# Kernel tuning notes

Measured on AMD Instinct MI355X. Metric: run time of the kernel, lower is better.

## Reference

```python
import jax, jax.numpy as jnp
import numpy as np

N_HEADS = 18
HEAD_DIM = 16
ROPE_THETA = 10000.0
SLIDING_WINDOW = 4096


def _rotate_half(x):
    half = x.shape[-1] // 2
    return jnp.concatenate([-x[..., half:], x[..., :half]], axis=-1)


def setup_inputs() -> dict:
    key = jax.random.key(0)
    k0, k1, k2, k3, k4 = jax.random.split(key, 5)
    B, S, H = 2, 2048, 288
    std = 0.02
    return {
        "hidden_states": jax.random.normal(k0, (B, S, H), dtype=jnp.float32),
        "Wq": jax.random.normal(k1, (H, H), dtype=jnp.float32) * std,
        "Wk": jax.random.normal(k2, (H, H), dtype=jnp.float32) * std,
        "Wv": jax.random.normal(k3, (H, H), dtype=jnp.float32) * std,
        "Wo": jax.random.normal(k4, (H, H), dtype=jnp.float32) * std,
    }


def reference(hidden_states, Wq, Wk, Wv, Wo):
    B, S, H = hidden_states.shape
    nH, D = N_HEADS, HEAD_DIM

    # QKV projections (nn.Linear: y = x @ W.T), reshape to [B, nH, S, D]
    def proj(W):
        return jnp.einsum("bsh,oh->bso", hidden_states, W).reshape(B, S, nH, D).transpose(0, 2, 1, 3)

    q, k, v = proj(Wq), proj(Wk), proj(Wv)

    # Rotary embedding: position_ids = arange(S)
    pos = jnp.arange(S, dtype=jnp.float32)
    inv_freq = 1.0 / (ROPE_THETA ** (jnp.arange(0, D, 2, dtype=jnp.float32) / D))
    freqs = pos[:, None] * inv_freq[None, :]            # [S, D/2]
    emb = jnp.concatenate([freqs, freqs], axis=-1)      # [S, D]
    cos = jnp.cos(emb)[None, None, :, :]                # [1, 1, S, D]
    sin = jnp.sin(emb)[None, None, :, :]
    q = q * cos + _rotate_half(q) * sin
    k = k * cos + _rotate_half(k) * sin

    # num_key_value_groups = 1 -> repeat_kv is identity.
    scores = jnp.einsum("bhqd,bhkd->bhqk", q, k) / jnp.sqrt(jnp.float32(D))

    # Sliding-window causal mask: attend iff 0 <= i - j < window
    i = jnp.arange(S)[:, None]
    j = jnp.arange(S)[None, :]
    allowed = (j <= i) & (i - j < SLIDING_WINDOW)       # [S, S]
    neg = jnp.finfo(scores.dtype).min
    scores = jnp.where(allowed[None, None, :, :], scores, neg)

    attn = jax.nn.softmax(scores.astype(jnp.float32), axis=-1).astype(q.dtype)
    out = jnp.einsum("bhqk,bhkd->bhqd", attn, v)        # [B, nH, S, D]
    out = out.transpose(0, 2, 1, 3).reshape(B, S, H)
    return jnp.einsum("bsh,oh->bso", out, Wo)
```

## Files before the change

kernel.cpp:

```cpp
#include <hip/hip_runtime.h>
#include <hip/hip_bf16.h>
#include <math.h>

#define H_DIM 288
#define NHEADS 18
#define HEAD_D 16
#define SEQ 2048
#define BATCH 2
#define M_TOT (BATCH*SEQ)
#define XCNT (M_TOT*H_DIM)
#define WCNT (H_DIM*H_DIM)

typedef _Float16 f16_t;
typedef __attribute__((ext_vector_type(4))) _Float16 half4v;
typedef __attribute__((ext_vector_type(8))) _Float16 half8v;
typedef __attribute__((ext_vector_type(4))) float   float4v;

__global__ __launch_bounds__(256) void cvt_f16(
    const float* __restrict__ X,
    const float* __restrict__ Wq, const float* __restrict__ Wk,
    const float* __restrict__ Wv, const float* __restrict__ Wo,
    f16_t* __restrict__ Xf, f16_t* __restrict__ Wf)
{
    int idx = blockIdx.x * 256 + threadIdx.x;
    const int X4 = XCNT/4, W4 = WCNT/4;
    if (idx >= X4 + 4*W4) return;
    const float* src; f16_t* dst; int off;
    if (idx < X4) { src = X; dst = Xf; off = idx; }
    else {
        int r = idx - X4;
        int wz = r / W4; off = r - wz*W4;
        src = (wz==0) ? Wq : (wz==1) ? Wk : (wz==2) ? Wv : Wo;
        dst = Wf + (size_t)wz*WCNT;
    }
    float4 v = ((const float4*)src)[off];
    half4v h; h[0]=(f16_t)v.x; h[1]=(f16_t)v.y; h[2]=(f16_t)v.z; h[3]=(f16_t)v.w;
    ((half4v*)dst)[off] = h;
}

__global__ __launch_bounds__(64) void qkv_mfma(
    const f16_t* __restrict__ Xf, const f16_t* __restrict__ Wf,
    f16_t* __restrict__ Q16, f16_t* __restrict__ K16, f16_t* __restrict__ Vt)
{
    const int bx = blockIdx.x;
    const int z  = bx/6;
    const int n0 = (bx - z*6)*48;
    const int m0 = blockIdx.y*32;
    const int lane = threadIdx.x & 63;
    const int n = lane & 15, quad = lane >> 4;

    const f16_t* W = Wf + (size_t)z*WCNT;

    float4v acc[2][3];
    #pragma unroll
    for (int mt = 0; mt < 2; mt++)
        #pragma unroll
        for (int nt = 0; nt < 3; nt++)
            acc[mt][nt] = (float4v){0.f,0.f,0.f,0.f};

    for (int k0 = 0; k0 < H_DIM; k0 += 32) {
        half8v a[2], b[3];
        #pragma unroll
        for (int mt = 0; mt < 2; mt++)
            a[mt] = *(const half8v*)(Xf + (size_t)(m0 + mt*16 + n)*H_DIM + k0 + quad*8);
        #pragma unroll
        for (int nt = 0; nt < 3; nt++)
            b[nt] = *(const half8v*)(W + (size_t)(n0 + nt*16 + n)*H_DIM + k0 + quad*8);
        #pragma unroll
        for (int mt = 0; mt < 2; mt++)
            #pragma unroll
            for (int nt = 0; nt < 3; nt++)
                acc[mt][nt] = __builtin_amdgcn_mfma_f32_16x16x32_f16(a[mt], b[nt], acc[mt][nt], 0, 0, 0);
    }

    if (z < 2) {
        f16_t* dst = (z == 0) ? Q16 : K16;
        const float invf = exp2f(-1.6609640474436813f * (float)(n & 7));
        #pragma unroll
        for (int mt = 0; mt < 2; mt++) {
            #pragma unroll
            for (int r = 0; r < 4; r++) {
                int m = m0 + mt*16 + quad*4 + r;
                int bb = m >> 11, s = m & (SEQ - 1);
                float ang = (float)s * invf;
                float c, sn;
                sincosf(ang, &sn, &c);
                #pragma unroll
                for (int nt = 0; nt < 3; nt++) {
                    float own = acc[mt][nt][r];
                    float par = __shfl_xor(own, 8, 64);
                    float val = (n & 8) ? fmaf(own, c, par*sn) : fmaf(own, c, -par*sn);
                    if (z == 0) val *= 0.25f;
                    int head = (n0 >> 4) + nt;
                    dst[((size_t)((bb*NHEADS + head)*SEQ) + s)*HEAD_D + n] = (f16_t)val;
                }
            }
        }
    } else {
        #pragma unroll
        for (int mt = 0; mt < 2; mt++)
            #pragma unroll
            for (int nt = 0; nt < 3; nt++)
                #pragma unroll
                for (int r = 0; r < 4; r++) {
                    int m = m0 + mt*16 + quad*4 + r;
                    int bb = m >> 11, s = m & (SEQ - 1);
                    int head = (n0 >> 4) + nt;
                    Vt[(size_t)(bb*NHEADS + head)*(SEQ*HEAD_D)
                       + (size_t)(s >> 4)*256 + n*16 + (s & 15)] = (f16_t)acc[mt][nt][r];
                }
    }
}

__global__ __launch_bounds__(256) void attn_mfma(
    const f16_t* __restrict__ Q16, const f16_t* __restrict__ K16,
    const f16_t* __restrict__ Vt, f16_t* __restrict__ Of)
{
    const int qp   = 63 - blockIdx.x;
    const int bh   = blockIdx.y;
    const int wave = threadIdx.x >> 6;
    const int lane = threadIdx.x & 63;
    const int n    = lane & 15;
    const int quad = lane >> 4;
    const int b = bh / NHEADS, h = bh - b*NHEADS;
    const int q0 = qp * 32;

    __shared__ float sacc[4][2][64][5];
    __shared__ float sl[4][2][64];

    half4v qb0 = *(const half4v*)(Q16 + ((size_t)bh*SEQ + q0 + n)*HEAD_D + quad*4);
    half4v qb1 = *(const half4v*)(Q16 + ((size_t)bh*SEQ + q0 + 16 + n)*HEAD_D + quad*4);
    const f16_t* Kb = K16 + (size_t)bh * SEQ * HEAD_D;
    const f16_t* Vb = Vt  + (size_t)bh * SEQ * HEAD_D;

    const float4v zero = {0.f, 0.f, 0.f, 0.f};
    float4v acc0 = zero, acc1 = zero;
    float l0 = 0.f, l1 = 0.f;

    const int ktmax = 2*qp + 1;
    int kt = wave;
    half4v ka, va;
    if (kt <= ktmax) {
        ka = *(const half4v*)(Kb + (size_t)(kt*16 + n)*HEAD_D + quad*4);
        va = *(const half4v*)(Vb + (size_t)kt*256 + n*16 + quad*4);
    }
    for (; kt <= ktmax; kt += 4) {
        half4v kan, van;
        if (kt + 4 <= ktmax) {
            kan = *(const half4v*)(Kb + (size_t)((kt+4)*16 + n)*HEAD_D + quad*4);
            van = *(const half4v*)(Vb + (size_t)(kt+4)*256 + n*16 + quad*4);
        }

        {
            float4v s = __builtin_amdgcn_mfma_f32_16x16x16f16(ka, qb1, zero, 0, 0, 0);
            float p[4];
            #pragma unroll
            for (int r = 0; r < 4; r++) {
                float e = __expf(s[r]);
                p[r] = (kt == ktmax && quad*4 + r > n) ? 0.0f : e;
            }
            l1 += (p[0] + p[1]) + (p[2] + p[3]);
            half4v pb;
            pb[0]=(f16_t)p[0]; pb[1]=(f16_t)p[1]; pb[2]=(f16_t)p[2]; pb[3]=(f16_t)p[3];
            acc1 = __builtin_amdgcn_mfma_f32_16x16x16f16(va, pb, acc1, 0, 0, 0);
        }
        if (kt < ktmax) {
            float4v s = __builtin_amdgcn_mfma_f32_16x16x16f16(ka, qb0, zero, 0, 0, 0);
            float p[4];
            #pragma unroll
            for (int r = 0; r < 4; r++) {
                float e = __expf(s[r]);
                p[r] = (kt == ktmax - 1 && quad*4 + r > n) ? 0.0f : e;
            }
            l0 += (p[0] + p[1]) + (p[2] + p[3]);
            half4v pb;
            pb[0]=(f16_t)p[0]; pb[1]=(f16_t)p[1]; pb[2]=(f16_t)p[2]; pb[3]=(f16_t)p[3];
            acc0 = __builtin_amdgcn_mfma_f32_16x16x16f16(va, pb, acc0, 0, 0, 0);
        }
        ka = kan; va = van;
    }

    #pragma unroll
    for (int r = 0; r < 4; r++) {
        sacc[wave][0][lane][r] = acc0[r];
        sacc[wave][1][lane][r] = acc1[r];
    }
    sl[wave][0][lane] = l0;
    sl[wave][1][lane] = l1;
    __syncthreads();

    if (wave < 2) {
        const int t = wave;
        float a[4] = {0.f, 0.f, 0.f, 0.f};
        float lsum = 0.f;
        #pragma unroll
        for (int w = 0; w < 4; w++) {
            lsum += sl[w][t][lane];
            #pragma unroll
            for (int r = 0; r < 4; r++) a[r] += sacc[w][t][lane][r];
        }
        lsum += __shfl_xor(lsum, 16, 64);
        lsum += __shfl_xor(lsum, 32, 64);
        float inv = 1.0f / lsum;
        half4v o;
        o[0]=(f16_t)(a[0]*inv); o[1]=(f16_t)(a[1]*inv);
        o[2]=(f16_t)(a[2]*inv); o[3]=(f16_t)(a[3]*inv);
        *(half4v*)(Of + (size_t)(b*SEQ + q0 + t*16 + n)*H_DIM + h*HEAD_D + quad*4) = o;
    }
}

__global__ __launch_bounds__(64) void out_mfma(
    const f16_t* __restrict__ Of, const f16_t* __restrict__ Wo16,
    float* __restrict__ C)
{
    const int n0 = blockIdx.x * 48;
    const int m0 = blockIdx.y * 32;
    const int lane = threadIdx.x & 63;
    const int n = lane & 15, quad = lane >> 4;

    float4v acc[2][3];
    #pragma unroll
    for (int mt = 0; mt < 2; mt++)
        #pragma unroll
        for (int nt = 0; nt < 3; nt++)
            acc[mt][nt] = (float4v){0.f,0.f,0.f,0.f};

    for (int k0 = 0; k0 < H_DIM; k0 += 32) {
        half8v a[2], b[3];
        #pragma unroll
        for (int mt = 0; mt < 2; mt++)
            a[mt] = *(const half8v*)(Of + (size_t)(m0 + mt*16 + n)*H_DIM + k0 + quad*8);
        #pragma unroll
        for (int nt = 0; nt < 3; nt++)
            b[nt] = *(const half8v*)(Wo16 + (size_t)(n0 + nt*16 + n)*H_DIM + k0 + quad*8);
        #pragma unroll
        for (int mt = 0; mt < 2; mt++)
            #pragma unroll
            for (int nt = 0; nt < 3; nt++)
                acc[mt][nt] = __builtin_amdgcn_mfma_f32_16x16x32_f16(a[mt], b[nt], acc[mt][nt], 0, 0, 0);
    }
    #pragma unroll
    for (int mt = 0; mt < 2; mt++)
        #pragma unroll
        for (int nt = 0; nt < 3; nt++)
            #pragma unroll
            for (int r = 0; r < 4; r++) {
                int m = m0 + mt*16 + quad*4 + r;
                C[(size_t)m*H_DIM + n0 + nt*16 + n] = acc[mt][nt][r];
            }
}

extern "C" void kernel_launch(void* const* d_in, const int* in_sizes, int n_in,
                              void* d_out, int out_size, void* d_ws, size_t ws_size,
                              hipStream_t stream)
{
    const float* Xh = (const float*)d_in[0];
    const float* Wq = (const float*)d_in[1];
    const float* Wk = (const float*)d_in[2];
    const float* Wv = (const float*)d_in[3];
    const float* Wo = (const float*)d_in[4];
    float* out = (float*)d_out;

    f16_t* Xf  = (f16_t*)d_ws;
    f16_t* Wf  = Xf + XCNT;
    f16_t* Q16 = Wf + 4*(size_t)WCNT;
    f16_t* K16 = Q16 + XCNT;
    f16_t* Vt  = K16 + XCNT;
    f16_t* Of  = Vt + XCNT;

    const int total4 = (XCNT + 4*WCNT)/4;
    cvt_f16<<<dim3((total4 + 255)/256), 256, 0, stream>>>(Xh, Wq, Wk, Wv, Wo, Xf, Wf);
    qkv_mfma<<<dim3(18, 128), 64, 0, stream>>>(Xf, Wf, Q16, K16, Vt);
    attn_mfma<<<dim3(64, 36), 256, 0, stream>>>(Q16, K16, Vt, Of);
    out_mfma<<<dim3(6, 128), 64, 0, stream>>>(Of, Wf + 3*(size_t)WCNT, out);
}
```

Measured before the change: 121.0 us.

## Fuse fp32-to-fp16 conversion into GEMMs and enlarge attention query tile

Removes the separate conversion kernel: the QKV and output projection kernels now load fp32 inputs and weights directly and convert them to fp16 in registers. The attention kernel now handles 64 query rows per block (four 16-row tiles) instead of 32, so each K/V tile load feeds four query tiles, and it launches half as many blocks. The shared-memory reduction layout is transposed to [r][lane]. This saves one launch and an intermediate round trip through memory, in exchange for twice the global load bytes for X and W in the GEMMs, plus more registers and fewer blocks in attention.

```diff
diff --git a/kernel.cpp b/kernel.cpp
--- a/kernel.cpp
+++ b/kernel.cpp
@@ -9,37 +9,22 @@
 #define BATCH 2
 #define M_TOT (BATCH*SEQ)
 #define XCNT (M_TOT*H_DIM)
-#define WCNT (H_DIM*H_DIM)
 
 typedef _Float16 f16_t;
 typedef __attribute__((ext_vector_type(4))) _Float16 half4v;
 typedef __attribute__((ext_vector_type(8))) _Float16 half8v;
 typedef __attribute__((ext_vector_type(4))) float   float4v;
 
-__global__ __launch_bounds__(256) void cvt_f16(
+__device__ __forceinline__ half8v f32x8_to_h8(float4 a, float4 b) {
+    half8v h;
+    h[0]=(f16_t)a.x; h[1]=(f16_t)a.y; h[2]=(f16_t)a.z; h[3]=(f16_t)a.w;
+    h[4]=(f16_t)b.x; h[5]=(f16_t)b.y; h[6]=(f16_t)b.z; h[7]=(f16_t)b.w;
+    return h;
+}
+
+__global__ __launch_bounds__(64) void qkv_mfma(
     const float* __restrict__ X,
-    const float* __restrict__ Wq, const float* __restrict__ Wk,
-    const float* __restrict__ Wv, const float* __restrict__ Wo,
-    f16_t* __restrict__ Xf, f16_t* __restrict__ Wf)
-{
-    int idx = blockIdx.x * 256 + threadIdx.x;
-    const int X4 = XCNT/4, W4 = WCNT/4;
-    if (idx >= X4 + 4*W4) return;
-    const float* src; f16_t* dst; int off;
-    if (idx < X4) { src = X; dst = Xf; off = idx; }
-    else {
-        int r = idx - X4;
-        int wz = r / W4; off = r - wz*W4;
-        src = (wz==0) ? Wq : (wz==1) ? Wk : (wz==2) ? Wv : Wo;
-        dst = Wf + (size_t)wz*WCNT;
-    }
-    float4 v = ((const float4*)src)[off];
-    half4v h; h[0]=(f16_t)v.x; h[1]=(f16_t)v.y; h[2]=(f16_t)v.z; h[3]=(f16_t)v.w;
-    ((half4v*)dst)[off] = h;
-}
-
-__global__ __launch_bounds__(64) void qkv_mfma(
-    const f16_t* __restrict__ Xf, const f16_t* __restrict__ Wf,
+    const float* __restrict__ Wq, const float* __restrict__ Wk, const float* __restrict__ Wv,
     f16_t* __restrict__ Q16, f16_t* __restrict__ K16, f16_t* __restrict__ Vt)
 {
     const int bx = blockIdx.x;
@@ -49,7 +34,7 @@
     const int lane = threadIdx.x & 63;
     const int n = lane & 15, quad = lane >> 4;
 
-    const f16_t* W = Wf + (size_t)z*WCNT;
+    const float* W = (z == 0) ? Wq : (z == 1) ? Wk : Wv;
 
     float4v acc[2][3];
     #pragma unroll
@@ -61,11 +46,15 @@
     for (int k0 = 0; k0 < H_DIM; k0 += 32) {
         half8v a[2], b[3];
         #pragma unroll
-        for (int mt = 0; mt < 2; mt++)
-            a[mt] = *(const half8v*)(Xf + (size_t)(m0 + mt*16 + n)*H_DIM + k0 + quad*8);
-        #pragma unroll
-        for (int nt = 0; nt < 3; nt++)
-            b[nt] = *(const half8v*)(W + (size_t)(n0 + nt*16 + n)*H_DIM + k0 + quad*8);
+        for (int mt = 0; mt < 2; mt++) {
+            const float4* p = (const float4*)(X + (size_t)(m0 + mt*16 + n)*H_DIM + k0 + quad*8);
+            a[mt] = f32x8_to_h8(p[0], p[1]);
+        }
+        #pragma unroll
+        for (int nt = 0; nt < 3; nt++) {
+            const float4* p = (const float4*)(W + (size_t)(n0 + nt*16 + n)*H_DIM + k0 + quad*8);
+            b[nt] = f32x8_to_h8(p[0], p[1]);
+        }
         #pragma unroll
         for (int mt = 0; mt < 2; mt++)
             #pragma unroll
@@ -116,28 +105,30 @@
     const f16_t* __restrict__ Q16, const f16_t* __restrict__ K16,
     const f16_t* __restrict__ Vt, f16_t* __restrict__ Of)
 {
-    const int qp   = 63 - blockIdx.x;
+    const int qp   = 31 - blockIdx.x;
     const int bh   = blockIdx.y;
     const int wave = threadIdx.x >> 6;
     const int lane = threadIdx.x & 63;
     const int n    = lane & 15;
     const int quad = lane >> 4;
     const int b = bh / NHEADS, h = bh - b*NHEADS;
-    const int q0 = qp * 32;
-
-    __shared__ float sacc[4][2][64][5];
-    __shared__ float sl[4][2][64];
-
-    half4v qb0 = *(const half4v*)(Q16 + ((size_t)bh*SEQ + q0 + n)*HEAD_D + quad*4);
-    half4v qb1 = *(const half4v*)(Q16 + ((size_t)bh*SEQ + q0 + 16 + n)*HEAD_D + quad*4);
+    const int q0 = qp * 64;
+
+    __shared__ float sacc[4][4][4][64];
+    __shared__ float sl[4][4][64];
+
+    half4v qb[4];
+    #pragma unroll
+    for (int t = 0; t < 4; t++)
+        qb[t] = *(const half4v*)(Q16 + ((size_t)bh*SEQ + q0 + t*16 + n)*HEAD_D + quad*4);
     const f16_t* Kb = K16 + (size_t)bh * SEQ * HEAD_D;
     const f16_t* Vb = Vt  + (size_t)bh * SEQ * HEAD_D;
 
     const float4v zero = {0.f, 0.f, 0.f, 0.f};
-    float4v acc0 = zero, acc1 = zero;
-    float l0 = 0.f, l1 = 0.f;
-
-    const int ktmax = 2*qp + 1;
+    float4v acc[4] = {zero, zero, zero, zero};
+    float l[4] = {0.f, 0.f, 0.f, 0.f};
+
+    const int ktmax = 4*qp + 3;
     int kt = wave;
     half4v ka, va;
     if (kt <= ktmax) {
@@ -150,46 +141,39 @@
             kan = *(const half4v*)(Kb + (size_t)((kt+4)*16 + n)*HEAD_D + quad*4);
             van = *(const half4v*)(Vb + (size_t)(kt+4)*256 + n*16 + quad*4);
         }
-
-        {
-            float4v s = __builtin_amdgcn_mfma_f32_16x16x16f16(ka, qb1, zero, 0, 0, 0);
+        #pragma unroll
+        for (int t = 0; t < 4; t++) {
+            const int lim = 4*qp + t;
+            if (kt > lim) continue;
+            float4v s = __builtin_amdgcn_mfma_f32_16x16x16f16(ka, qb[t], zero, 0, 0, 0);
             float p[4];
-            #pragma unroll
-            for (int r = 0; r < 4; r++) {
-                float e = __expf(s[r]);
-                p[r] = (kt == ktmax && quad*4 + r > n) ? 0.0f : e;
+            if (kt == lim) {
+                #pragma unroll
+                for (int r = 0; r < 4; r++) {
+                    float e = __expf(s[r]);
+                    p[r] = (quad*4 + r <= n) ? e : 0.0f;
+                }
+            } else {
+                #pragma unroll
+                for (int r = 0; r < 4; r++) p[r] = __expf(s[r]);
             }
-            l1 += (p[0] + p[1]) + (p[2] + p[3]);
+            l[t] += (p[0] + p[1]) + (p[2] + p[3]);
             half4v pb;
             pb[0]=(f16_t)p[0]; pb[1]=(f16_t)p[1]; pb[2]=(f16_t)p[2]; pb[3]=(f16_t)p[3];
-            acc1 = __builtin_amdgcn_mfma_f32_16x16x16f16(va, pb, acc1, 0, 0, 0);
-        }
-        if (kt < ktmax) {
-            float4v s = __builtin_amdgcn_mfma_f32_16x16x16f16(ka, qb0, zero, 0, 0, 0);
-            float p[4];
-            #pragma unroll
-            for (int r = 0; r < 4; r++) {
-                float e = __expf(s[r]);
-                p[r] = (kt == ktmax - 1 && quad*4 + r > n) ? 0.0f : e;
-            }
-            l0 += (p[0] + p[1]) + (p[2] + p[3]);
-            half4v pb;
-            pb[0]=(f16_t)p[0]; pb[1]=(f16_t)p[1]; pb[2]=(f16_t)p[2]; pb[3]=(f16_t)p[3];
-            acc0 = __builtin_amdgcn_mfma_f32_16x16x16f16(va, pb, acc0, 0, 0, 0);
+            acc[t] = __builtin_amdgcn_mfma_f32_16x16x16f16(va, pb, acc[t], 0, 0, 0);
         }
         ka = kan; va = van;
     }
 
     #pragma unroll
-    for (int r = 0; r < 4; r++) {
-        sacc[wave][0][lane][r] = acc0[r];
-        sacc[wave][1][lane][r] = acc1[r];
-    }
-    sl[wave][0][lane] = l0;
-    sl[wave][1][lane] = l1;
+    for (int t = 0; t < 4; t++) {
+        #pragma unroll
+        for (int r = 0; r < 4; r++) sacc[wave][t][r][lane] = acc[t][r];
+        sl[wave][t][lane] = l[t];
+    }
     __syncthreads();
 
-    if (wave < 2) {
+    {
         const int t = wave;
         float a[4] = {0.f, 0.f, 0.f, 0.f};
         float lsum = 0.f;
@@ -197,7 +181,7 @@
         for (int w = 0; w < 4; w++) {
             lsum += sl[w][t][lane];
             #pragma unroll
-            for (int r = 0; r < 4; r++) a[r] += sacc[w][t][lane][r];
+            for (int r = 0; r < 4; r++) a[r] += sacc[w][t][r][lane];
         }
         lsum += __shfl_xor(lsum, 16, 64);
         lsum += __shfl_xor(lsum, 32, 64);
@@ -210,7 +194,7 @@
 }
 
 __global__ __launch_bounds__(64) void out_mfma(
-    const f16_t* __restrict__ Of, const f16_t* __restrict__ Wo16,
+    const f16_t* __restrict__ Of, const float* __restrict__ Wo,
     float* __restrict__ C)
 {
     const int n0 = blockIdx.x * 48;
@@ -231,8 +215,10 @@
         for (int mt = 0; mt < 2; mt++)
             a[mt] = *(const half8v*)(Of + (size_t)(m0 + mt*16 + n)*H_DIM + k0 + quad*8);
         #pragma unroll
-        for (int nt = 0; nt < 3; nt++)
-            b[nt] = *(const half8v*)(Wo16 + (size_t)(n0 + nt*16 + n)*H_DIM + k0 + quad*8);
+        for (int nt = 0; nt < 3; nt++) {
+            const float4* p = (const float4*)(Wo + (size_t)(n0 + nt*16 + n)*H_DIM + k0 + quad*8);
+            b[nt] = f32x8_to_h8(p[0], p[1]);
+        }
         #pragma unroll
         for (int mt = 0; mt < 2; mt++)
             #pragma unroll
@@ -261,16 +247,12 @@
     const float* Wo = (const float*)d_in[4];
     float* out = (float*)d_out;
 
-    f16_t* Xf  = (f16_t*)d_ws;
-    f16_t* Wf  = Xf + XCNT;
-    f16_t* Q16 = Wf + 4*(size_t)WCNT;
+    f16_t* Q16 = (f16_t*)d_ws;
     f16_t* K16 = Q16 + XCNT;
     f16_t* Vt  = K16 + XCNT;
     f16_t* Of  = Vt + XCNT;
 
-    const int total4 = (XCNT + 4*WCNT)/4;
-    cvt_f16<<<dim3((total4 + 255)/256), 256, 0, stream>>>(Xh, Wq, Wk, Wv, Wo, Xf, Wf);
-    qkv_mfma<<<dim3(18, 128), 64, 0, stream>>>(Xf, Wf, Q16, K16, Vt);
-    attn_mfma<<<dim3(64, 36), 256, 0, stream>>>(Q16, K16, Vt, Of);
-    out_mfma<<<dim3(6, 128), 64, 0, stream>>>(Of, Wf + 3*(size_t)WCNT, out);
-}
+    qkv_mfma<<<dim3(18, 128), 64, 0, stream>>>(Xh, Wq, Wk, Wv, Q16, K16, Vt);
+    attn_mfma<<<dim3(32, 36), 256, 0, stream>>>(Q16, K16, Vt, Of);
+    out_mfma<<<dim3(6, 128), 64, 0, stream>>>(Of, Wo, out);
+}
```

Result: slower. 150.1 us (+24.1%).

## Split attention into fixed-size key chunks with separate reduction kernel

Applied to the files above, without the earlier changes.

Replaces the per-query-block attention kernel, where four waves stride over keys and reduce through shared memory, with a split-K scheme. Each wave now handles one chunk of up to 16 key tiles for one 32-query block, giving balanced work units; a second kernel sums the partial accumulators and row sums and normalises. It also folds log2(e) into the Q scale so the hardware exp2 can replace expf. The cost is an extra launch and global round-trips for the partial sums.

```diff
diff --git a/kernel.cpp b/kernel.cpp
--- a/kernel.cpp
+++ b/kernel.cpp
@@ -10,6 +10,8 @@
 #define M_TOT (BATCH*SEQ)
 #define XCNT (M_TOT*H_DIM)
 #define WCNT (H_DIM*H_DIM)
+#define NUNITS 10368
+#define NQUNITS 2304
 
 typedef _Float16 f16_t;
 typedef __attribute__((ext_vector_type(4))) _Float16 half4v;
@@ -90,7 +92,7 @@
                     float own = acc[mt][nt][r];
                     float par = __shfl_xor(own, 8, 64);
                     float val = (n & 8) ? fmaf(own, c, par*sn) : fmaf(own, c, -par*sn);
-                    if (z == 0) val *= 0.25f;
+                    if (z == 0) val *= 0.36067376022224085f;
                     int head = (n0 >> 4) + nt;
                     dst[((size_t)((bb*NHEADS + head)*SEQ) + s)*HEAD_D + n] = (f16_t)val;
                 }
@@ -112,21 +114,30 @@
     }
 }
 
-__global__ __launch_bounds__(256) void attn_mfma(
+__global__ __launch_bounds__(256) void attn_part(
     const f16_t* __restrict__ Q16, const f16_t* __restrict__ K16,
-    const f16_t* __restrict__ Vt, f16_t* __restrict__ Of)
-{
-    const int qp   = 63 - blockIdx.x;
-    const int bh   = blockIdx.y;
-    const int wave = threadIdx.x >> 6;
+    const f16_t* __restrict__ Vt,
+    float4* __restrict__ accbuf, float* __restrict__ lbuf)
+{
+    const int unit = blockIdx.x*4 + (threadIdx.x >> 6);
     const int lane = threadIdx.x & 63;
-    const int n    = lane & 15;
-    const int quad = lane >> 4;
-    const int b = bh / NHEADS, h = bh - b*NHEADS;
-    const int q0 = qp * 32;
-
-    __shared__ float sacc[4][2][64][5];
-    __shared__ float sl[4][2][64];
+    const int n = lane & 15, quad = lane >> 4;
+
+    const int bh = unit / 288;
+    const int rem = unit - bh*288;
+    int g, t0;
+    if      (rem < 8)   { g=0; t0=rem;     }
+    else if (rem < 24)  { g=1; t0=rem-8;   }
+    else if (rem < 48)  { g=2; t0=rem-24;  }
+    else if (rem < 80)  { g=3; t0=rem-48;  }
+    else if (rem < 120) { g=4; t0=rem-80;  }
+    else if (rem < 168) { g=5; t0=rem-120; }
+    else if (rem < 224) { g=6; t0=rem-168; }
+    else                { g=7; t0=rem-224; }
+    const int qd = t0 / (g+1);
+    const int qp = 8*g + qd;
+    const int chunk = t0 - qd*(g+1);
+    const int q0 = qp*32;
 
     half4v qb0 = *(const half4v*)(Q16 + ((size_t)bh*SEQ + q0 + n)*HEAD_D + quad*4);
     half4v qb1 = *(const half4v*)(Q16 + ((size_t)bh*SEQ + q0 + 16 + n)*HEAD_D + quad*4);
@@ -137,40 +148,39 @@
     float4v acc0 = zero, acc1 = zero;
     float l0 = 0.f, l1 = 0.f;
 
-    const int ktmax = 2*qp + 1;
-    int kt = wave;
-    half4v ka, va;
-    if (kt <= ktmax) {
-        ka = *(const half4v*)(Kb + (size_t)(kt*16 + n)*HEAD_D + quad*4);
-        va = *(const half4v*)(Vb + (size_t)kt*256 + n*16 + quad*4);
-    }
-    for (; kt <= ktmax; kt += 4) {
+    const int lim0 = 2*qp, lim1 = 2*qp + 1;
+    const int ktlo = chunk*16;
+    const int kthi = min(ktlo + 15, lim1);
+
+    int kt = ktlo;
+    half4v ka = *(const half4v*)(Kb + (size_t)(kt*16 + n)*HEAD_D + quad*4);
+    half4v va = *(const half4v*)(Vb + (size_t)kt*256 + n*16 + quad*4);
+    for (; kt <= kthi; kt++) {
         half4v kan, van;
-        if (kt + 4 <= ktmax) {
-            kan = *(const half4v*)(Kb + (size_t)((kt+4)*16 + n)*HEAD_D + quad*4);
-            van = *(const half4v*)(Vb + (size_t)(kt+4)*256 + n*16 + quad*4);
-        }
-
+        if (kt < kthi) {
+            kan = *(const half4v*)(Kb + (size_t)((kt+1)*16 + n)*HEAD_D + quad*4);
+            van = *(const half4v*)(Vb + (size_t)(kt+1)*256 + n*16 + quad*4);
+        }
         {
             float4v s = __builtin_amdgcn_mfma_f32_16x16x16f16(ka, qb1, zero, 0, 0, 0);
             float p[4];
             #pragma unroll
             for (int r = 0; r < 4; r++) {
-                float e = __expf(s[r]);
-                p[r] = (kt == ktmax && quad*4 + r > n) ? 0.0f : e;
+                float e = __builtin_amdgcn_exp2f(s[r]);
+                p[r] = (kt == lim1 && quad*4 + r > n) ? 0.0f : e;
             }
             l1 += (p[0] + p[1]) + (p[2] + p[3]);
             half4v pb;
             pb[0]=(f16_t)p[0]; pb[1]=(f16_t)p[1]; pb[2]=(f16_t)p[2]; pb[3]=(f16_t)p[3];
             acc1 = __builtin_amdgcn_mfma_f32_16x16x16f16(va, pb, acc1, 0, 0, 0);
         }
-        if (kt < ktmax) {
+        if (kt <= lim0) {
             float4v s = __builtin_amdgcn_mfma_f32_16x16x16f16(ka, qb0, zero, 0, 0, 0);
             float p[4];
             #pragma unroll
             for (int r = 0; r < 4; r++) {
-                float e = __expf(s[r]);
-                p[r] = (kt == ktmax - 1 && quad*4 + r > n) ? 0.0f : e;
+                float e = __builtin_amdgcn_exp2f(s[r]);
+                p[r] = (kt == lim0 && quad*4 + r > n) ? 0.0f : e;
             }
             l0 += (p[0] + p[1]) + (p[2] + p[3]);
             half4v pb;
@@ -180,32 +190,44 @@
         ka = kan; va = van;
     }
 
+    float4 a0; a0.x=acc0[0]; a0.y=acc0[1]; a0.z=acc0[2]; a0.w=acc0[3];
+    float4 a1; a1.x=acc1[0]; a1.y=acc1[1]; a1.z=acc1[2]; a1.w=acc1[3];
+    accbuf[((size_t)unit*2 + 0)*64 + lane] = a0;
+    accbuf[((size_t)unit*2 + 1)*64 + lane] = a1;
+    lbuf[((size_t)unit*2 + 0)*64 + lane] = l0;
+    lbuf[((size_t)unit*2 + 1)*64 + lane] = l1;
+}
+
+__global__ __launch_bounds__(256) void attn_red(
+    const float4* __restrict__ accbuf, const float* __restrict__ lbuf,
+    f16_t* __restrict__ Of)
+{
+    const int wid = blockIdx.x*4 + (threadIdx.x >> 6);
+    const int lane = threadIdx.x & 63;
+    const int n = lane & 15, quad = lane >> 4;
+    const int bh = wid >> 6, qp = wid & 63;
+    const int b = bh / NHEADS, h = bh - b*NHEADS;
+    const int g = qp >> 3, j = qp & 7;
+    const int nch = g + 1;
+    const int ubase = bh*288 + qp + 4*g*(g-1) + g*j;
+
     #pragma unroll
-    for (int r = 0; r < 4; r++) {
-        sacc[wave][0][lane][r] = acc0[r];
-        sacc[wave][1][lane][r] = acc1[r];
-    }
-    sl[wave][0][lane] = l0;
-    sl[wave][1][lane] = l1;
-    __syncthreads();
-
-    if (wave < 2) {
-        const int t = wave;
-        float a[4] = {0.f, 0.f, 0.f, 0.f};
-        float lsum = 0.f;
-        #pragma unroll
-        for (int w = 0; w < 4; w++) {
-            lsum += sl[w][t][lane];
-            #pragma unroll
-            for (int r = 0; r < 4; r++) a[r] += sacc[w][t][lane][r];
-        }
-        lsum += __shfl_xor(lsum, 16, 64);
-        lsum += __shfl_xor(lsum, 32, 64);
-        float inv = 1.0f / lsum;
+    for (int t = 0; t < 2; t++) {
+        float4 a = {0.f, 0.f, 0.f, 0.f};
+        float l = 0.f;
+        for (int c = 0; c < nch; c++) {
+            size_t idx = ((size_t)(ubase + c)*2 + t)*64 + lane;
+            float4 v = accbuf[idx];
+            a.x += v.x; a.y += v.y; a.z += v.z; a.w += v.w;
+            l += lbuf[idx];
+        }
+        l += __shfl_xor(l, 16, 64);
+        l += __shfl_xor(l, 32, 64);
+        float inv = 1.0f / l;
         half4v o;
-        o[0]=(f16_t)(a[0]*inv); o[1]=(f16_t)(a[1]*inv);
-        o[2]=(f16_t)(a[2]*inv); o[3]=(f16_t)(a[3]*inv);
-        *(half4v*)(Of + (size_t)(b*SEQ + q0 + t*16 + n)*H_DIM + h*HEAD_D + quad*4) = o;
+        o[0]=(f16_t)(a.x*inv); o[1]=(f16_t)(a.y*inv);
+        o[2]=(f16_t)(a.z*inv); o[3]=(f16_t)(a.w*inv);
+        *(half4v*)(Of + (size_t)(b*SEQ + qp*32 + t*16 + n)*H_DIM + h*HEAD_D + quad*4) = o;
     }
 }
 
@@ -267,10 +289,13 @@
     f16_t* K16 = Q16 + XCNT;
     f16_t* Vt  = K16 + XCNT;
     f16_t* Of  = Vt + XCNT;
+    float4* accbuf = (float4*)(Of + XCNT);
+    float*  lbuf   = (float*)(accbuf + (size_t)NUNITS*2*64);
 
     const int total4 = (XCNT + 4*WCNT)/4;
     cvt_f16<<<dim3((total4 + 255)/256), 256, 0, stream>>>(Xh, Wq, Wk, Wv, Wo, Xf, Wf);
     qkv_mfma<<<dim3(18, 128), 64, 0, stream>>>(Xf, Wf, Q16, K16, Vt);
-    attn_mfma<<<dim3(64, 36), 256, 0, stream>>>(Q16, K16, Vt, Of);
+    attn_part<<<dim3(NUNITS/4), 256, 0, stream>>>(Q16, K16, Vt, accbuf, lbuf);
+    attn_red<<<dim3(NQUNITS/4), 256, 0, stream>>>(accbuf, lbuf, Of);
     out_mfma<<<dim3(6, 128), 64, 0, stream>>>(Of, Wf + 3*(size_t)WCNT, out);
 }
```

New measurement: 116.6 us. 1.04x faster.
